# Kernel optimization log

Hardware: AMD Instinct MI355X
Metric: run time of the kernel (lower is better)

Reference implementation:

```python
import jax, jax.numpy as jnp
import numpy as np

B, S, D, H = 4, 2048, 1024, 16
HD = D // H  # head_dim = 64


def setup_inputs() -> dict:
    key = jax.random.key(0)
    ks = jax.random.split(key, 5)
    scale = 1.0 / np.sqrt(D)
    return {
        "x": jax.random.normal(ks[0], (B, S, D), dtype=jnp.float32),
        "Wq": jax.random.normal(ks[1], (D, D), dtype=jnp.float32) * scale,
        "bq": jnp.zeros((D,), dtype=jnp.float32),
        "Wk": jax.random.normal(ks[2], (D, D), dtype=jnp.float32) * scale,
        "bk": jnp.zeros((D,), dtype=jnp.float32),
        "Wv": jax.random.normal(ks[3], (D, D), dtype=jnp.float32) * scale,
        "bv": jnp.zeros((D,), dtype=jnp.float32),
        "Wo": jax.random.normal(ks[4], (D, D), dtype=jnp.float32) * scale,
        "bo": jnp.zeros((D,), dtype=jnp.float32),
    }


def reference(x, Wq, bq, Wk, bk, Wv, bv, Wo, bo):
    # Linear layers (torch Linear: y = x @ W^T + b)
    q = jnp.einsum("bsd,ed->bse", x, Wq) + bq
    k = jnp.einsum("bsd,ed->bse", x, Wk) + bk
    v = jnp.einsum("bsd,ed->bse", x, Wv) + bv
    # split heads -> [B, H, S, HD]
    q = q.reshape(B, S, H, HD).transpose(0, 2, 1, 3)
    k = k.reshape(B, S, H, HD).transpose(0, 2, 1, 3)
    v = v.reshape(B, S, H, HD).transpose(0, 2, 1, 3)
    # NOTE: original scales by 1/sqrt(d_model), not 1/sqrt(head_dim)
    scores = jnp.einsum("bhqd,bhkd->bhqk", q, k) / jnp.sqrt(jnp.float32(D))
    causal = jnp.tril(jnp.ones((S, S), dtype=bool))
    scores = jnp.where(causal, scores, -jnp.inf)
    probs = jax.nn.softmax(scores, axis=-1)  # dropout p=0 -> identity
    attn = jnp.einsum("bhqk,bhkd->bhqd", probs, v)
    # merge heads -> [B, S, D]
    attn = attn.transpose(0, 2, 1, 3).reshape(B, S, D)
    out = jnp.einsum("bsd,ed->bse", attn, Wo) + bo
    return out
```

## Files before the change

kernel.cpp:

```cpp
#include <hip/hip_runtime.h>
#include <hip/hip_bf16.h>
#include <stdint.h>
#include <stddef.h>

#define B_N 4
#define S_N 2048
#define D_N 1024
#define H_N 16
#define HD_N 64

typedef __bf16 bf16;
typedef __bf16 bf16x8 __attribute__((ext_vector_type(8)));
typedef __bf16 bf16x4 __attribute__((ext_vector_type(4)));
typedef float f32x4 __attribute__((ext_vector_type(4)));

__device__ __forceinline__ void gload_lds16(const void* g, void* l) {
  __builtin_amdgcn_global_load_lds((const __attribute__((address_space(1))) void*)g,
                                   (__attribute__((address_space(3))) void*)l,
                                   16, 0, 0);
}

__global__ __launch_bounds__(256) void cvt_f32_bf16(const float* __restrict__ in,
                                                    bf16* __restrict__ out, int n4) {
  int i = blockIdx.x * blockDim.x + threadIdx.x;
  const int stride = gridDim.x * blockDim.x;
  for (; i < n4; i += stride) {
    const float4 v = ((const float4*)in)[i];
    bf16x4 o;
    o[0] = (bf16)v.x; o[1] = (bf16)v.y; o[2] = (bf16)v.z; o[3] = (bf16)v.w;
    ((bf16x4*)out)[i] = o;
  }
}

__global__ __launch_bounds__(256) void cvt_w4(const float* __restrict__ w0,
                                              const float* __restrict__ w1,
                                              const float* __restrict__ w2,
                                              const float* __restrict__ w3,
                                              bf16* __restrict__ o0, bf16* __restrict__ o1,
                                              bf16* __restrict__ o2, bf16* __restrict__ o3) {
  const int n4 = (D_N * D_N) / 4;
  const int which = blockIdx.x >> 9;
  const float* in = which == 0 ? w0 : which == 1 ? w1 : which == 2 ? w2 : w3;
  bf16* out = which == 0 ? o0 : which == 1 ? o1 : which == 2 ? o2 : o3;
  int i = (blockIdx.x & 511) * 256 + threadIdx.x;
  const int stride = 512 * 256;
  for (; i < n4; i += stride) {
    const float4 v = ((const float4*)in)[i];
    bf16x4 o;
    o[0] = (bf16)v.x; o[1] = (bf16)v.y; o[2] = (bf16)v.z; o[3] = (bf16)v.w;
    ((bf16x4*)out)[i] = o;
  }
}

__global__ __launch_bounds__(512, 2) void gemm_qkv3(const bf16* __restrict__ A,
                                                    const bf16* __restrict__ Wq,
                                                    const bf16* __restrict__ Wk,
                                                    const bf16* __restrict__ Wv,
                                                    const float* __restrict__ bq,
                                                    const float* __restrict__ bk,
                                                    const float* __restrict__ bv,
                                                    bf16* __restrict__ outQ,
                                                    bf16* __restrict__ outK,
                                                    bf16* __restrict__ outVt) {
  __shared__ __align__(16) char smem[3 * 40960];
  const int tid = threadIdx.x;
  const int wid = tid >> 6;
  const int lane = tid & 63;
  const int l16 = lane & 15;
  const int lhi = lane >> 4;
  const int n0 = blockIdx.x * 128;
  const int m0 = blockIdx.y * 256;

  const int wm = (wid >> 1) * 64;
  const int wn = (wid & 1) * 64;
  const int srow4 = lane >> 2;
  const int scol = 8 * ((lane & 3) ^ (srow4 & 3));
  const int rswz = ((lhi ^ (l16 & 3)) * 16);

  f32x4 acc[3][4][4];
#pragma unroll
  for (int w = 0; w < 3; ++w)
#pragma unroll
    for (int i = 0; i < 4; ++i)
#pragma unroll
      for (int j = 0; j < 4; ++j) acc[w][i][j] = (f32x4){0.f, 0.f, 0.f, 0.f};

#define STG(buf_, kt_)                                                                   \
  {                                                                                      \
    _Pragma("unroll") for (int q = 0; q < 2; ++q)                                        \
        gload_lds16(A + (size_t)(m0 + q * 128 + wid * 16 + srow4) * D_N + (kt_)*32 + scol, \
                    smem + (buf_)*40960 + q * 8192 + wid * 1024);                        \
    gload_lds16(Wq + (size_t)(n0 + wid * 16 + srow4) * D_N + (kt_)*32 + scol,            \
                smem + (buf_)*40960 + 16384 + wid * 1024);                               \
    gload_lds16(Wk + (size_t)(n0 + wid * 16 + srow4) * D_N + (kt_)*32 + scol,            \
                smem + (buf_)*40960 + 16384 + 8192 + wid * 1024);                        \
    gload_lds16(Wv + (size_t)(n0 + wid * 16 + srow4) * D_N + (kt_)*32 + scol,            \
                smem + (buf_)*40960 + 16384 + 16384 + wid * 1024);                       \
  }

#define PHASE(buf_)                                                                      \
  {                                                                                      \
    const char* a_ = smem + (buf_)*40960;                                                \
    const char* b_ = a_ + 16384;                                                         \
    bf16x8 af[4];                                                                        \
    _Pragma("unroll") for (int i = 0; i < 4; ++i)                                        \
        af[i] = *(const bf16x8*)(a_ + (wm + i * 16 + l16) * 64 + rswz);                  \
    _Pragma("unroll") for (int w = 0; w < 3; ++w) {                                      \
      bf16x8 bfr[4];                                                                     \
      _Pragma("unroll") for (int j = 0; j < 4; ++j)                                      \
          bfr[j] = *(const bf16x8*)(b_ + (w * 128 + wn + j * 16 + l16) * 64 + rswz);     \
      __builtin_amdgcn_s_setprio(1);                                                     \
      _Pragma("unroll") for (int i = 0; i < 4; ++i)                                      \
          _Pragma("unroll") for (int j = 0; j < 4; ++j)                                  \
              acc[w][i][j] = __builtin_amdgcn_mfma_f32_16x16x32_bf16(af[i], bfr[j],      \
                                                                     acc[w][i][j], 0, 0, 0); \
      __builtin_amdgcn_s_setprio(0);                                                     \
    }                                                                                    \
  }

  const int NT = D_N / 32;

  STG(0, 0);
  STG(1, 1);
  asm volatile("s_waitcnt vmcnt(5)" ::: "memory");
  asm volatile("s_barrier" ::: "memory");

  for (int t = 0; t < NT - 2; ++t) {
    STG((t + 2) % 3, t + 2);
    PHASE(t % 3);
    asm volatile("s_waitcnt vmcnt(5) lgkmcnt(0)" ::: "memory");
    asm volatile("s_barrier" ::: "memory");
  }
  PHASE((NT - 2) % 3);
  asm volatile("s_waitcnt vmcnt(0) lgkmcnt(0)" ::: "memory");
  asm volatile("s_barrier" ::: "memory");
  PHASE((NT - 1) % 3);

#undef STG
#undef PHASE

#pragma unroll
  for (int w = 0; w < 3; ++w) {
    const float* bias = w == 0 ? bq : w == 1 ? bk : bv;
#pragma unroll
    for (int i = 0; i < 4; ++i) {
#pragma unroll
      for (int j = 0; j < 4; ++j) {
        const int row0 = m0 + wm + i * 16 + lhi * 4;
        const int col = n0 + wn + j * 16 + l16;
        const float bvv = bias[col];
        const int h = col >> 6, hd = col & 63;
        if (w == 2) {
          const int b = row0 >> 11, s = row0 & (S_N - 1);
          bf16x4 pk;
#pragma unroll
          for (int r = 0; r < 4; ++r) pk[r] = (bf16)(acc[w][i][j][r] + bvv);
          *(bf16x4*)&outVt[(((size_t)b * H_N + h) * HD_N + hd) * S_N + s] = pk;
        } else {
          bf16* out = w == 0 ? outQ : outK;
#pragma unroll
          for (int r = 0; r < 4; ++r) {
            const int row = row0 + r;
            const int b = row >> 11, s = row & (S_N - 1);
            out[(((size_t)b * H_N + h) * S_N + s) * HD_N + hd] = (bf16)(acc[w][i][j][r] + bvv);
          }
        }
      }
    }
  }
}

template <typename OutFn>
__device__ __forceinline__ void gemm_body(const bf16* __restrict__ A,
                                          const bf16* __restrict__ W, int m0, int n0,
                                          bf16* sAq, bf16* sBq, OutFn&& emit) {
  const int tid = threadIdx.x;
  const int wave = tid >> 6;
  const int lane = tid & 63;
  const int l16 = lane & 15;
  const int lhi = lane >> 4;
  const int wm = (wave >> 1) * 64;
  const int wn = (wave & 1) * 64;
  const int srow = wave * 8 + (lane >> 3);
  const int scol = 8 * ((lane & 7) ^ (lane >> 3));
  const int sdst = wave * 8 * 64;
  const int aoff0 = (lhi ^ (l16 & 7)) * 8;

  f32x4 acc[4][4];
#pragma unroll
  for (int i = 0; i < 4; ++i)
#pragma unroll
    for (int j = 0; j < 4; ++j) acc[i][j] = (f32x4){0.f, 0.f, 0.f, 0.f};

#define SG_A(buf_, kt_)                                                                 \
  {                                                                                     \
    _Pragma("unroll") for (int q = 0; q < 4; ++q)                                       \
        gload_lds16(A + (size_t)(m0 + q * 64 + srow) * D_N + (kt_) * 64 + scol,         \
                    sAq + (buf_) * 16384 + sdst + q * 4096);                            \
  }
#define SG_B(buf_, kt_)                                                                 \
  {                                                                                     \
    _Pragma("unroll") for (int q = 0; q < 2; ++q)                                       \
        gload_lds16(W + (size_t)(n0 + q * 64 + srow) * D_N + (kt_) * 64 + scol,         \
                    sBq + (buf_) * 8192 + sdst + q * 4096);                             \
  }
#define PHASE(cur_, kk_)                                                                \
  {                                                                                     \
    const bf16* a_ = sAq + (cur_) * 16384;                                              \
    const bf16* b_ = sBq + (cur_) * 8192;                                               \
    bf16x8 af[4], bfr[4];                                                               \
    _Pragma("unroll") for (int i = 0; i < 4; ++i)                                       \
        af[i] = *(const bf16x8*)(a_ + (wm + i * 16 + l16) * 64 + (aoff0 ^ ((kk_)*32))); \
    _Pragma("unroll") for (int j = 0; j < 4; ++j)                                       \
        bfr[j] = *(const bf16x8*)(b_ + (wn + j * 16 + l16) * 64 + (aoff0 ^ ((kk_)*32)));\
    __builtin_amdgcn_s_setprio(1);                                                      \
    _Pragma("unroll") for (int i = 0; i < 4; ++i)                                       \
        _Pragma("unroll") for (int j = 0; j < 4; ++j)                                   \
            acc[i][j] = __builtin_amdgcn_mfma_f32_16x16x32_bf16(af[i], bfr[j],          \
                                                                acc[i][j], 0, 0, 0);    \
    __builtin_amdgcn_s_setprio(0);                                                      \
  }

  const int NT = D_N / 64;

  SG_A(0, 0); SG_B(0, 0);
  SG_A(1, 1); SG_B(1, 1);
  asm volatile("s_waitcnt vmcnt(6)" ::: "memory");
  asm volatile("s_barrier" ::: "memory");

  for (int t = 0; t < NT - 2; ++t) {
    const int cur = t % 3, nx = (t + 2) % 3;
    SG_A(nx, t + 2);
    PHASE(cur, 0);
    SG_B(nx, t + 2);
    PHASE(cur, 1);
    asm volatile("s_waitcnt vmcnt(6) lgkmcnt(0)" ::: "memory");
    asm volatile("s_barrier" ::: "memory");
  }
  PHASE((NT - 2) % 3, 0);
  PHASE((NT - 2) % 3, 1);
  asm volatile("s_waitcnt vmcnt(0) lgkmcnt(0)" ::: "memory");
  asm volatile("s_barrier" ::: "memory");
  PHASE((NT - 1) % 3, 0);
  PHASE((NT - 1) % 3, 1);

#undef SG_A
#undef SG_B
#undef PHASE

#pragma unroll
  for (int i = 0; i < 4; ++i)
#pragma unroll
    for (int j = 0; j < 4; ++j)
      emit(m0 + wm + i * 16 + lhi * 4, n0 + wn + j * 16 + l16, acc[i][j]);
}

__global__ __launch_bounds__(512) void gemm_out(const bf16* __restrict__ A,
                                                const bf16* __restrict__ W,
                                                const float* __restrict__ bias,
                                                float* __restrict__ out) {
  __shared__ __align__(16) bf16 sAq[3 * 256 * 64];
  __shared__ __align__(16) bf16 sBq[3 * 128 * 64];
  const int n0 = blockIdx.x * 128;
  const int m0 = blockIdx.y * 256;
  gemm_body(A, W, m0, n0, sAq, sBq, [&](int row0, int col, const f32x4& a) {
    const float bvv = bias[col];
#pragma unroll
    for (int r = 0; r < 4; ++r) out[(size_t)(row0 + r) * D_N + col] = a[r] + bvv;
  });
}

__global__ __launch_bounds__(256, 3) void attn_fwd(const bf16* __restrict__ Q,
                                                   const bf16* __restrict__ K,
                                                   const bf16* __restrict__ Vt,
                                                   bf16* __restrict__ O) {
  __shared__ __align__(16) bf16 sK[2][64 * 64];
  __shared__ __align__(16) bf16 sV[2][64 * 64];
  __shared__ __align__(16) bf16 sP[4][32 * 72];
  const int tid = threadIdx.x;
  const int wave = tid >> 6;
  const int lane = tid & 63;
  const int l16 = lane & 15;
  const int lhi = lane >> 4;
  const int bidx = blockIdx.x;
  const int bh = bidx & 63;
  const int qt = 15 - (bidx >> 6);
  const int q0 = qt * 128 + wave * 32;
  const bf16* Qh = Q + (size_t)bh * S_N * HD_N;
  const bf16* Kh = K + (size_t)bh * S_N * HD_N;
  const bf16* Vth = Vt + (size_t)bh * HD_N * S_N;
  const int b = bh >> 4, h = bh & 15;

  const int srow = lane >> 3;
  const int scol = 8 * ((lane & 7) ^ srow);

  const float QS = 0.03125f * 1.44269504088896340736f;
  const f32x4 z4 = {0.0f, 0.0f, 0.0f, 0.0f};
  const f32x4 m4 = {-4.0f, -4.0f, -4.0f, -4.0f};
  const bf16 oneb = (bf16)1.0f;
  const bf16x8 ones = {oneb, oneb, oneb, oneb, oneb, oneb, oneb, oneb};
  bf16* sPw = sP[wave];

  bf16x8 qf[2][2];
#pragma unroll
  for (int i = 0; i < 2; ++i)
#pragma unroll
    for (int kq = 0; kq < 2; ++kq) {
      const bf16x8 raw =
          *(const bf16x8*)&Qh[(size_t)(q0 + i * 16 + l16) * HD_N + kq * 32 + lhi * 8];
      bf16x8 s;
#pragma unroll
      for (int e = 0; e < 8; ++e) s[e] = (bf16)((float)raw[e] * QS);
      qf[i][kq] = s;
    }

  f32x4 o[2][4];
  f32x4 osum[2];
#pragma unroll
  for (int i = 0; i < 2; ++i) {
#pragma unroll
    for (int j = 0; j < 4; ++j) o[i][j] = z4;
    osum[i] = z4;
  }

#define STAGE(buf, kb_)                                                                  \
  {                                                                                      \
    _Pragma("unroll") for (int is = 0; is < 2; ++is) {                                   \
      const int r0 = is * 32 + wave * 8;                                                 \
      gload_lds16(Kh + (size_t)((kb_)*64 + r0 + srow) * HD_N + scol, &sK[buf][r0 * 64]); \
      gload_lds16(Vth + (size_t)(r0 + srow) * S_N + (kb_)*64 + scol, &sV[buf][r0 * 64]); \
    }                                                                                    \
  }

  const int nkb = 2 * qt + 2;

  STAGE(0, 0);
  __syncthreads();

  for (int kb = 0; kb < nkb; ++kb) {
    const int cur = kb & 1;
    if (kb + 1 < nkb) STAGE(cur ^ 1, kb + 1);
    const bf16* sKb = sK[cur];
    const bf16* sVb = sV[cur];
    const int k0 = kb * 64;

    if (k0 <= q0 + 31) {
      f32x4 sc[2][4];
#pragma unroll
      for (int i = 0; i < 2; ++i)
#pragma unroll
        for (int j = 0; j < 4; ++j) sc[i][j] = m4;
      __builtin_amdgcn_s_setprio(1);
#pragma unroll
      for (int j = 0; j < 4; ++j) {
        const int row = j * 16 + l16;
#pragma unroll
        for (int kq = 0; kq < 2; ++kq) {
          const bf16x8 kfr = *(const bf16x8*)((const char*)sKb + row * 128 +
                                              ((kq * 64 + lhi * 16) ^ ((row & 7) << 4)));
#pragma unroll
          for (int i = 0; i < 2; ++i)
            sc[i][j] = __builtin_amdgcn_mfma_f32_16x16x32_bf16(qf[i][kq], kfr, sc[i][j], 0, 0, 0);
        }
      }
      __builtin_amdgcn_s_setprio(0);

      if (k0 + 63 > q0) {
#pragma unroll
        for (int i = 0; i < 2; ++i)
#pragma unroll
          for (int r = 0; r < 4; ++r) {
            const int qrow = q0 + i * 16 + lhi * 4 + r;
#pragma unroll
            for (int j = 0; j < 4; ++j)
              if (k0 + j * 16 + l16 > qrow) sc[i][j][r] = -3e38f;
          }
      }

#pragma unroll
      for (int i = 0; i < 2; ++i)
#pragma unroll
        for (int r = 0; r < 4; ++r)
#pragma unroll
          for (int j = 0; j < 4; ++j)
            sPw[(i * 16 + lhi * 4 + r) * 72 + j * 16 + l16] =
                (bf16)__builtin_amdgcn_exp2f(sc[i][j][r]);

      __builtin_amdgcn_s_setprio(1);
#pragma unroll
      for (int kq = 0; kq < 2; ++kq) {
        bf16x8 pa[2];
#pragma unroll
        for (int i = 0; i < 2; ++i)
          pa[i] = *(const bf16x8*)&sPw[(i * 16 + l16) * 72 + kq * 32 + lhi * 8];
#pragma unroll
        for (int i = 0; i < 2; ++i)
          osum[i] = __builtin_amdgcn_mfma_f32_16x16x32_bf16(pa[i], ones, osum[i], 0, 0, 0);
#pragma unroll
        for (int jd = 0; jd < 4; ++jd) {
          const int vrow = jd * 16 + l16;
          const bf16x8 vb = *(const bf16x8*)((const char*)sVb + vrow * 128 +
                                             ((kq * 64 + lhi * 16) ^ ((vrow & 7) << 4)));
#pragma unroll
          for (int i = 0; i < 2; ++i)
            o[i][jd] = __builtin_amdgcn_mfma_f32_16x16x32_bf16(pa[i], vb, o[i][jd], 0, 0, 0);
        }
      }
      __builtin_amdgcn_s_setprio(0);
    }
    __syncthreads();
  }

#pragma unroll
  for (int i = 0; i < 2; ++i) {
#pragma unroll
    for (int r = 0; r < 4; ++r) {
      const float inv = __builtin_amdgcn_rcpf(osum[i][r]);
      const size_t token = (size_t)b * S_N + q0 + i * 16 + lhi * 4 + r;
#pragma unroll
      for (int jd = 0; jd < 4; ++jd) {
        const int col = h * 64 + jd * 16 + l16;
        O[token * D_N + col] = (bf16)(o[i][jd][r] * inv);
      }
    }
  }
#undef STAGE
}

extern "C" void kernel_launch(void* const* d_in, const int* in_sizes, int n_in,
                              void* d_out, int out_size, void* d_ws, size_t ws_size,
                              hipStream_t stream) {
  const float* x  = (const float*)d_in[0];
  const float* Wq = (const float*)d_in[1];
  const float* bq = (const float*)d_in[2];
  const float* Wk = (const float*)d_in[3];
  const float* bk = (const float*)d_in[4];
  const float* Wv = (const float*)d_in[5];
  const float* bv = (const float*)d_in[6];
  const float* Wo = (const float*)d_in[7];
  const float* bo = (const float*)d_in[8];

  char* ws = (char*)d_ws;
  const size_t MB = 1u << 20;
  bf16* xb  = (bf16*)(ws);
  bf16* qB  = (bf16*)(ws + 16 * MB);
  bf16* kB  = (bf16*)(ws + 32 * MB);
  bf16* vtB = (bf16*)(ws + 48 * MB);
  bf16* wqb = (bf16*)(ws + 64 * MB);
  bf16* wkb = (bf16*)(ws + 66 * MB);
  bf16* wvb = (bf16*)(ws + 68 * MB);
  bf16* wob = (bf16*)(ws + 70 * MB);

  cvt_f32_bf16<<<2048, 256, 0, stream>>>(x, xb, (B_N * S_N * D_N) / 4);
  cvt_w4<<<2048, 256, 0, stream>>>(Wq, Wk, Wv, Wo, wqb, wkb, wvb, wob);

  gemm_qkv3<<<dim3(8, 32), 512, 0, stream>>>(xb, wqb, wkb, wvb, bq, bk, bv, qB, kB, vtB);

  attn_fwd<<<dim3(1024), 256, 0, stream>>>(qB, kB, vtB, xb);

  gemm_out<<<dim3(8, 32), 512, 0, stream>>>(xb, wob, bo, (float*)d_out);
}
```

Measured before the change: 158.0 us.

## Shrink GEMM tiles to 128x128 with 4 waves and double buffering

Both the QKV projection and output GEMMs drop from 256x128 tiles with 8 waves and triple-buffered LDS to 128x128 tiles with 4 waves and double-buffered LDS. The launch grid doubles to 512 blocks, and gemm_out moves to a K-step of 32 with the same swizzle as the QKV kernel. The aim is better occupancy and load balance across CUs by using more, smaller blocks with less LDS each. The cost is less operand reuse per tile, and the barrier sits before the next stage is issued, which reduces overlap of loads with MFMA work.

```diff
diff --git a/kernel.cpp b/kernel.cpp
--- a/kernel.cpp
+++ b/kernel.cpp
@@ -52,7 +52,7 @@
   }
 }
 
-__global__ __launch_bounds__(512, 2) void gemm_qkv3(const bf16* __restrict__ A,
+__global__ __launch_bounds__(256, 2) void gemm_qkv3(const bf16* __restrict__ A,
                                                     const bf16* __restrict__ Wq,
                                                     const bf16* __restrict__ Wk,
                                                     const bf16* __restrict__ Wv,
@@ -62,20 +62,20 @@
                                                     bf16* __restrict__ outQ,
                                                     bf16* __restrict__ outK,
                                                     bf16* __restrict__ outVt) {
-  __shared__ __align__(16) char smem[3 * 40960];
+  __shared__ __align__(16) char smem[2 * 32768];
   const int tid = threadIdx.x;
   const int wid = tid >> 6;
   const int lane = tid & 63;
   const int l16 = lane & 15;
   const int lhi = lane >> 4;
   const int n0 = blockIdx.x * 128;
-  const int m0 = blockIdx.y * 256;
+  const int m0 = blockIdx.y * 128;
 
   const int wm = (wid >> 1) * 64;
   const int wn = (wid & 1) * 64;
   const int srow4 = lane >> 2;
   const int scol = 8 * ((lane & 3) ^ (srow4 & 3));
-  const int rswz = ((lhi ^ (l16 & 3)) * 16);
+  const int rswz = (lhi ^ (l16 & 3)) * 16;
 
   f32x4 acc[3][4][4];
 #pragma unroll
@@ -85,56 +85,60 @@
 #pragma unroll
       for (int j = 0; j < 4; ++j) acc[w][i][j] = (f32x4){0.f, 0.f, 0.f, 0.f};
 
-#define STG(buf_, kt_)                                                                   \
-  {                                                                                      \
-    _Pragma("unroll") for (int q = 0; q < 2; ++q)                                        \
-        gload_lds16(A + (size_t)(m0 + q * 128 + wid * 16 + srow4) * D_N + (kt_)*32 + scol, \
-                    smem + (buf_)*40960 + q * 8192 + wid * 1024);                        \
-    gload_lds16(Wq + (size_t)(n0 + wid * 16 + srow4) * D_N + (kt_)*32 + scol,            \
-                smem + (buf_)*40960 + 16384 + wid * 1024);                               \
-    gload_lds16(Wk + (size_t)(n0 + wid * 16 + srow4) * D_N + (kt_)*32 + scol,            \
-                smem + (buf_)*40960 + 16384 + 8192 + wid * 1024);                        \
-    gload_lds16(Wv + (size_t)(n0 + wid * 16 + srow4) * D_N + (kt_)*32 + scol,            \
-                smem + (buf_)*40960 + 16384 + 16384 + wid * 1024);                       \
-  }
-
-#define PHASE(buf_)                                                                      \
-  {                                                                                      \
-    const char* a_ = smem + (buf_)*40960;                                                \
-    const char* b_ = a_ + 16384;                                                         \
-    bf16x8 af[4];                                                                        \
-    _Pragma("unroll") for (int i = 0; i < 4; ++i)                                        \
-        af[i] = *(const bf16x8*)(a_ + (wm + i * 16 + l16) * 64 + rswz);                  \
-    _Pragma("unroll") for (int w = 0; w < 3; ++w) {                                      \
-      bf16x8 bfr[4];                                                                     \
-      _Pragma("unroll") for (int j = 0; j < 4; ++j)                                      \
-          bfr[j] = *(const bf16x8*)(b_ + (w * 128 + wn + j * 16 + l16) * 64 + rswz);     \
-      __builtin_amdgcn_s_setprio(1);                                                     \
-      _Pragma("unroll") for (int i = 0; i < 4; ++i)                                      \
-          _Pragma("unroll") for (int j = 0; j < 4; ++j)                                  \
-              acc[w][i][j] = __builtin_amdgcn_mfma_f32_16x16x32_bf16(af[i], bfr[j],      \
+#define STG(buf_, kt_)                                                                    \
+  {                                                                                       \
+    _Pragma("unroll") for (int q = 0; q < 2; ++q)                                         \
+        gload_lds16(A + (size_t)(m0 + q * 64 + wid * 16 + srow4) * D_N + (kt_)*32 + scol, \
+                    smem + (buf_)*32768 + q * 4096 + wid * 1024);                         \
+    _Pragma("unroll") for (int q = 0; q < 2; ++q) {                                       \
+      gload_lds16(Wq + (size_t)(n0 + q * 64 + wid * 16 + srow4) * D_N + (kt_)*32 + scol,  \
+                  smem + (buf_)*32768 + 8192 + q * 4096 + wid * 1024);                    \
+      gload_lds16(Wk + (size_t)(n0 + q * 64 + wid * 16 + srow4) * D_N + (kt_)*32 + scol,  \
+                  smem + (buf_)*32768 + 16384 + q * 4096 + wid * 1024);                   \
+      gload_lds16(Wv + (size_t)(n0 + q * 64 + wid * 16 + srow4) * D_N + (kt_)*32 + scol,  \
+                  smem + (buf_)*32768 + 24576 + q * 4096 + wid * 1024);                   \
+    }                                                                                     \
+  }
+
+#define PHASE(buf_)                                                                       \
+  {                                                                                       \
+    const char* a_ = smem + (buf_)*32768;                                                 \
+    const char* b_ = a_ + 8192;                                                           \
+    bf16x8 af[4];                                                                         \
+    _Pragma("unroll") for (int i = 0; i < 4; ++i)                                         \
+        af[i] = *(const bf16x8*)(a_ + (wm + i * 16 + l16) * 64 + rswz);                   \
+    _Pragma("unroll") for (int w = 0; w < 3; ++w) {                                       \
+      bf16x8 bfr[4];                                                                      \
+      _Pragma("unroll") for (int j = 0; j < 4; ++j)                                       \
+          bfr[j] = *(const bf16x8*)(b_ + (w * 128 + wn + j * 16 + l16) * 64 + rswz);      \
+      __builtin_amdgcn_s_setprio(1);                                                      \
+      _Pragma("unroll") for (int i = 0; i < 4; ++i)                                       \
+          _Pragma("unroll") for (int j = 0; j < 4; ++j)                                   \
+              acc[w][i][j] = __builtin_amdgcn_mfma_f32_16x16x32_bf16(af[i], bfr[j],       \
                                                                      acc[w][i][j], 0, 0, 0); \
-      __builtin_amdgcn_s_setprio(0);                                                     \
-    }                                                                                    \
+      __builtin_amdgcn_s_setprio(0);                                                      \
+    }                                                                                     \
   }
 
   const int NT = D_N / 32;
 
   STG(0, 0);
   STG(1, 1);
-  asm volatile("s_waitcnt vmcnt(5)" ::: "memory");
+  asm volatile("s_waitcnt vmcnt(8)" ::: "memory");
   asm volatile("s_barrier" ::: "memory");
 
   for (int t = 0; t < NT - 2; ++t) {
-    STG((t + 2) % 3, t + 2);
-    PHASE(t % 3);
-    asm volatile("s_waitcnt vmcnt(5) lgkmcnt(0)" ::: "memory");
+    const int cur = t & 1;
+    PHASE(cur);
     asm volatile("s_barrier" ::: "memory");
-  }
-  PHASE((NT - 2) % 3);
-  asm volatile("s_waitcnt vmcnt(0) lgkmcnt(0)" ::: "memory");
+    STG(cur, t + 2);
+    asm volatile("s_waitcnt vmcnt(8)" ::: "memory");
+    asm volatile("s_barrier" ::: "memory");
+  }
+  PHASE(0);
+  asm volatile("s_waitcnt vmcnt(0)" ::: "memory");
   asm volatile("s_barrier" ::: "memory");
-  PHASE((NT - 1) % 3);
+  PHASE(1);
 
 #undef STG
 #undef PHASE
@@ -170,21 +174,24 @@
   }
 }
 
-template <typename OutFn>
-__device__ __forceinline__ void gemm_body(const bf16* __restrict__ A,
-                                          const bf16* __restrict__ W, int m0, int n0,
-                                          bf16* sAq, bf16* sBq, OutFn&& emit) {
+__global__ __launch_bounds__(256, 3) void gemm_out(const bf16* __restrict__ A,
+                                                   const bf16* __restrict__ W,
+                                                   const float* __restrict__ bias,
+                                                   float* __restrict__ out) {
+  __shared__ __align__(16) char smem[2 * 16384];
   const int tid = threadIdx.x;
-  const int wave = tid >> 6;
+  const int wid = tid >> 6;
   const int lane = tid & 63;
   const int l16 = lane & 15;
   const int lhi = lane >> 4;
-  const int wm = (wave >> 1) * 64;
-  const int wn = (wave & 1) * 64;
-  const int srow = wave * 8 + (lane >> 3);
-  const int scol = 8 * ((lane & 7) ^ (lane >> 3));
-  const int sdst = wave * 8 * 64;
-  const int aoff0 = (lhi ^ (l16 & 7)) * 8;
+  const int n0 = blockIdx.x * 128;
+  const int m0 = blockIdx.y * 128;
+
+  const int wm = (wid >> 1) * 64;
+  const int wn = (wid & 1) * 64;
+  const int srow4 = lane >> 2;
+  const int scol = 8 * ((lane & 3) ^ (srow4 & 3));
+  const int rswz = (lhi ^ (l16 & 3)) * 16;
 
   f32x4 acc[4][4];
 #pragma unroll
@@ -192,82 +199,67 @@
 #pragma unroll
     for (int j = 0; j < 4; ++j) acc[i][j] = (f32x4){0.f, 0.f, 0.f, 0.f};
 
-#define SG_A(buf_, kt_)                                                                 \
-  {                                                                                     \
-    _Pragma("unroll") for (int q = 0; q < 4; ++q)                                       \
-        gload_lds16(A + (size_t)(m0 + q * 64 + srow) * D_N + (kt_) * 64 + scol,         \
-                    sAq + (buf_) * 16384 + sdst + q * 4096);                            \
-  }
-#define SG_B(buf_, kt_)                                                                 \
-  {                                                                                     \
-    _Pragma("unroll") for (int q = 0; q < 2; ++q)                                       \
-        gload_lds16(W + (size_t)(n0 + q * 64 + srow) * D_N + (kt_) * 64 + scol,         \
-                    sBq + (buf_) * 8192 + sdst + q * 4096);                             \
-  }
-#define PHASE(cur_, kk_)                                                                \
-  {                                                                                     \
-    const bf16* a_ = sAq + (cur_) * 16384;                                              \
-    const bf16* b_ = sBq + (cur_) * 8192;                                               \
-    bf16x8 af[4], bfr[4];                                                               \
-    _Pragma("unroll") for (int i = 0; i < 4; ++i)                                       \
-        af[i] = *(const bf16x8*)(a_ + (wm + i * 16 + l16) * 64 + (aoff0 ^ ((kk_)*32))); \
-    _Pragma("unroll") for (int j = 0; j < 4; ++j)                                       \
-        bfr[j] = *(const bf16x8*)(b_ + (wn + j * 16 + l16) * 64 + (aoff0 ^ ((kk_)*32)));\
-    __builtin_amdgcn_s_setprio(1);                                                      \
-    _Pragma("unroll") for (int i = 0; i < 4; ++i)                                       \
-        _Pragma("unroll") for (int j = 0; j < 4; ++j)                                   \
-            acc[i][j] = __builtin_amdgcn_mfma_f32_16x16x32_bf16(af[i], bfr[j],          \
-                                                                acc[i][j], 0, 0, 0);    \
-    __builtin_amdgcn_s_setprio(0);                                                      \
-  }
-
-  const int NT = D_N / 64;
-
-  SG_A(0, 0); SG_B(0, 0);
-  SG_A(1, 1); SG_B(1, 1);
-  asm volatile("s_waitcnt vmcnt(6)" ::: "memory");
+#define STG(buf_, kt_)                                                                    \
+  {                                                                                       \
+    _Pragma("unroll") for (int q = 0; q < 2; ++q) {                                       \
+      gload_lds16(A + (size_t)(m0 + q * 64 + wid * 16 + srow4) * D_N + (kt_)*32 + scol,   \
+                  smem + (buf_)*16384 + q * 4096 + wid * 1024);                           \
+      gload_lds16(W + (size_t)(n0 + q * 64 + wid * 16 + srow4) * D_N + (kt_)*32 + scol,   \
+                  smem + (buf_)*16384 + 8192 + q * 4096 + wid * 1024);                    \
+    }                                                                                     \
+  }
+
+#define PHASE(buf_)                                                                       \
+  {                                                                                       \
+    const char* a_ = smem + (buf_)*16384;                                                 \
+    const char* b_ = a_ + 8192;                                                           \
+    bf16x8 af[4], bfr[4];                                                                 \
+    _Pragma("unroll") for (int i = 0; i < 4; ++i)                                         \
+        af[i] = *(const bf16x8*)(a_ + (wm + i * 16 + l16) * 64 + rswz);                   \
+    _Pragma("unroll") for (int j = 0; j < 4; ++j)                                         \
+        bfr[j] = *(const bf16x8*)(b_ + (wn + j * 16 + l16) * 64 + rswz);                  \
+    __builtin_amdgcn_s_setprio(1);                                                        \
+    _Pragma("unroll") for (int i = 0; i < 4; ++i)                                         \
+        _Pragma("unroll") for (int j = 0; j < 4; ++j)                                     \
+            acc[i][j] = __builtin_amdgcn_mfma_f32_16x16x32_bf16(af[i], bfr[j],            \
+                                                                acc[i][j], 0, 0, 0);      \
+    __builtin_amdgcn_s_setprio(0);                                                        \
+  }
+
+  const int NT = D_N / 32;
+
+  STG(0, 0);
+  STG(1, 1);
+  asm volatile("s_waitcnt vmcnt(4)" ::: "memory");
   asm volatile("s_barrier" ::: "memory");
 
   for (int t = 0; t < NT - 2; ++t) {
-    const int cur = t % 3, nx = (t + 2) % 3;
-    SG_A(nx, t + 2);
-    PHASE(cur, 0);
-    SG_B(nx, t + 2);
-    PHASE(cur, 1);
-    asm volatile("s_waitcnt vmcnt(6) lgkmcnt(0)" ::: "memory");
+    const int cur = t & 1;
+    PHASE(cur);
     asm volatile("s_barrier" ::: "memory");
-  }
-  PHASE((NT - 2) % 3, 0);
-  PHASE((NT - 2) % 3, 1);
-  asm volatile("s_waitcnt vmcnt(0) lgkmcnt(0)" ::: "memory");
+    STG(cur, t + 2);
+    asm volatile("s_waitcnt vmcnt(4)" ::: "memory");
+    asm volatile("s_barrier" ::: "memory");
+  }
+  PHASE(0);
+  asm volatile("s_waitcnt vmcnt(0)" ::: "memory");
   asm volatile("s_barrier" ::: "memory");
-  PHASE((NT - 1) % 3, 0);
-  PHASE((NT - 1) % 3, 1);
-
-#undef SG_A
-#undef SG_B
+  PHASE(1);
+
+#undef STG
 #undef PHASE
 
 #pragma unroll
-  for (int i = 0; i < 4; ++i)
-#pragma unroll
-    for (int j = 0; j < 4; ++j)
-      emit(m0 + wm + i * 16 + lhi * 4, n0 + wn + j * 16 + l16, acc[i][j]);
-}
-
-__global__ __launch_bounds__(512) void gemm_out(const bf16* __restrict__ A,
-                                                const bf16* __restrict__ W,
-                                                const float* __restrict__ bias,
-                                                float* __restrict__ out) {
-  __shared__ __align__(16) bf16 sAq[3 * 256 * 64];
-  __shared__ __align__(16) bf16 sBq[3 * 128 * 64];
-  const int n0 = blockIdx.x * 128;
-  const int m0 = blockIdx.y * 256;
-  gemm_body(A, W, m0, n0, sAq, sBq, [&](int row0, int col, const f32x4& a) {
-    const float bvv = bias[col];
-#pragma unroll
-    for (int r = 0; r < 4; ++r) out[(size_t)(row0 + r) * D_N + col] = a[r] + bvv;
-  });
+  for (int i = 0; i < 4; ++i) {
+#pragma unroll
+    for (int j = 0; j < 4; ++j) {
+      const int row0 = m0 + wm + i * 16 + lhi * 4;
+      const int col = n0 + wn + j * 16 + l16;
+      const float bvv = bias[col];
+#pragma unroll
+      for (int r = 0; r < 4; ++r) out[(size_t)(row0 + r) * D_N + col] = acc[i][j][r] + bvv;
+    }
+  }
 }
 
 __global__ __launch_bounds__(256, 3) void attn_fwd(const bf16* __restrict__ Q,
@@ -454,9 +446,9 @@
   cvt_f32_bf16<<<2048, 256, 0, stream>>>(x, xb, (B_N * S_N * D_N) / 4);
   cvt_w4<<<2048, 256, 0, stream>>>(Wq, Wk, Wv, Wo, wqb, wkb, wvb, wob);
 
-  gemm_qkv3<<<dim3(8, 32), 512, 0, stream>>>(xb, wqb, wkb, wvb, bq, bk, bv, qB, kB, vtB);
+  gemm_qkv3<<<dim3(8, 64), 256, 0, stream>>>(xb, wqb, wkb, wvb, bq, bk, bv, qB, kB, vtB);
 
   attn_fwd<<<dim3(1024), 256, 0, stream>>>(qB, kB, vtB, xb);
 
-  gemm_out<<<dim3(8, 32), 512, 0, stream>>>(xb, wob, bo, (float*)d_out);
-}
+  gemm_out<<<dim3(8, 64), 256, 0, stream>>>(xb, wob, bo, (float*)d_out);
+}
```

Result: no change. 155.0 us (-1.9%).
